# Performance work log

Measured on AMD Instinct MI355X. Metric: run time of the kernel, lower is better.

The kernel has to match this reference:

```python
import jax, jax.numpy as jnp
import numpy as np

SPAN = 20
REPEAT = 90


def setup_inputs() -> dict:
    key = jax.random.key(0)
    k1, k2 = jax.random.split(key)
    B, C, H, W = 4, 1, 512, 512
    pred = jax.random.normal(k1, (B, C, H, W), dtype=jnp.float32)
    gt = jax.random.normal(k2, (B, C, H, W), dtype=jnp.float32)
    # random offsets: magnitude in [1, span], random sign (matches np.random logic in torch module)
    rng = np.random.default_rng(0)
    mag_h = rng.integers(1, SPAN + 1, size=REPEAT)
    mag_w = rng.integers(1, SPAN + 1, size=REPEAT)
    sign_h = np.where(rng.uniform(size=REPEAT) > 0.5, -1, 1)
    sign_w = np.where(rng.uniform(size=REPEAT) > 0.5, -1, 1)
    h_offsets = jnp.asarray(mag_h * sign_h, dtype=jnp.int32)
    w_offsets = jnp.asarray(mag_w * sign_w, dtype=jnp.int32)
    return {"pred": pred, "gt": gt, "h_offsets": h_offsets, "w_offsets": w_offsets}


def _relative_depth(x, h_offsets, w_offsets):
    """x: [B,C,H,W] -> [B,Hb,Wb,R*C] stack of base-block minus shifted-block diffs."""
    B, C, H, W = x.shape
    Hb, Wb = H - 2 * SPAN, W - 2 * SPAN
    base = jax.lax.dynamic_slice(x, (0, 0, SPAN, SPAN), (B, C, Hb, Wb))

    def one_shift(h, w):
        shifted = jax.lax.dynamic_slice(x, (0, 0, SPAN + h, SPAN + w), (B, C, Hb, Wb))
        return base - shifted

    rd = jax.vmap(one_shift)(h_offsets, w_offsets)          # [R,B,C,Hb,Wb]
    R = rd.shape[0]
    rd = jnp.transpose(rd, (1, 0, 2, 3, 4)).reshape(B, R * C, Hb, Wb)  # concat along channel
    return jnp.transpose(rd, (0, 2, 3, 1))                   # [B,Hb,Wb,R*C]


def _l2_normalize(rd):
    norm = jnp.linalg.norm(rd, axis=-1, keepdims=True)
    norm = jnp.where(norm == 0, jnp.ones_like(norm), norm)
    return rd / norm


def reference(pred, gt, h_offsets, w_offsets):
    pred_rd = _l2_normalize(_relative_depth(pred, h_offsets, w_offsets))
    gt_rd = _l2_normalize(_relative_depth(gt, h_offsets, w_offsets))
    return jnp.mean(jnp.abs(pred_rd - gt_rd))
```

## Files before the change

kernel.cpp:

```cpp
#include <hip/hip_runtime.h>
#include <hip/hip_fp16.h>

#define SPAN 20
#define REPEAT 90


constexpr int W  = 512;
constexpr int Wb = 472;
constexpr int TJ = 64;
constexpr int TI = 8;
constexpr int TW = TJ + 2 * SPAN;
constexpr int TH = TI + 2 * SPAN;

__global__ __launch_bounds__(256) void rd_loss_kernel(
    const float* __restrict__ pred, const float* __restrict__ gt,
    const int* __restrict__ hoff, const int* __restrict__ woff,
    float* __restrict__ out)
{
    __shared__ __half2 tile[TH * TW];
    __shared__ float wsum[4];

    const int t  = threadIdx.x;
    const int bx = blockIdx.x;
    const int by = blockIdx.y;
    const int b  = blockIdx.z;
    const int I0 = by * TI;
    const int J0 = bx * TJ;

    const float* pb_ = pred + b * (W * W);
    const float* gb_ = gt   + b * (W * W);

    for (int e = t; e < TH * TW; e += 256) {
        const int row = e / TW;
        const int col = e - row * TW;
        const int gr  = I0 + row;
        int gc        = J0 + col; gc = gc < 511 ? gc : 511;
        const int gi  = gr * W + gc;
        tile[e] = __floats2half2_rn(pb_[gi], gb_[gi]);
    }
    __syncthreads();

    const int jp = t & 31;
    const int ii = t >> 5;
    const int jj = 2 * jp;
    const int j0 = J0 + jj;

    const int base0 = (SPAN + ii) * TW + (SPAN + jj);
    const __half2 c0 = tile[base0];
    const __half2 c1 = tile[base0 + 1];

    __half2 d0[REPEAT], d1[REPEAT];
    __half2 sA0 = __floats2half2_rn(0.f, 0.f), sB0 = sA0;
    __half2 sA1 = sA0, sB1 = sA0;
    #pragma unroll
    for (int r = 0; r < REPEAT; ++r) {
        const int off = hoff[r] * TW + woff[r];
        const __half2 v0 = tile[base0 + off];
        const __half2 v1 = tile[base0 + off + 1];
        d0[r] = __hsub2(c0, v0);
        d1[r] = __hsub2(c1, v1);
        if (r & 1) { sB0 = __hfma2(d0[r], d0[r], sB0); sB1 = __hfma2(d1[r], d1[r], sB1); }
        else       { sA0 = __hfma2(d0[r], d0[r], sA0); sA1 = __hfma2(d1[r], d1[r], sA1); }
    }
    const float ssp0 = __half2float(__low2half(sA0))  + __half2float(__low2half(sB0));
    const float ssg0 = __half2float(__high2half(sA0)) + __half2float(__high2half(sB0));
    const float ssp1 = __half2float(__low2half(sA1))  + __half2float(__low2half(sB1));
    const float ssg1 = __half2float(__high2half(sA1)) + __half2float(__high2half(sB1));

    const float invp0 = (ssp0 == 0.f) ? 1.f : rsqrtf(ssp0);
    const float invg0 = (ssg0 == 0.f) ? 1.f : rsqrtf(ssg0);
    const float invp1 = (ssp1 == 0.f) ? 1.f : rsqrtf(ssp1);
    const float invg1 = (ssg1 == 0.f) ? 1.f : rsqrtf(ssg1);

    const __half nr0 = __float2half(-(invg0 / invp0));
    const __half nr1 = __float2half(-(invg1 / invp1));

    __half aA0 = __float2half(0.f), aB0 = aA0, aA1 = aA0, aB1 = aA0;
    #pragma unroll
    for (int r = 0; r < REPEAT; ++r) {
        const __half s0 = __hfma(nr0, __high2half(d0[r]), __low2half(d0[r]));
        const __half s1 = __hfma(nr1, __high2half(d1[r]), __low2half(d1[r]));
        if (r & 1) { aB0 = __hadd(aB0, __habs(s0)); aB1 = __hadd(aB1, __habs(s1)); }
        else       { aA0 = __hadd(aA0, __habs(s0)); aA1 = __hadd(aA1, __habs(s1)); }
    }
    const float l0 = invp0 * (__half2float(aA0) + __half2float(aB0));
    const float l1 = invp1 * (__half2float(aA1) + __half2float(aB1));

    float lsum = ((j0 < Wb) ? l0 : 0.f) + ((j0 + 1 < Wb) ? l1 : 0.f);

    #pragma unroll
    for (int o = 32; o > 0; o >>= 1) lsum += __shfl_down(lsum, o, 64);

    const int lane = t & 63;
    const int wid  = t >> 6;
    if (lane == 0) wsum[wid] = lsum;
    __syncthreads();

    if (t == 0) {
        const float s = wsum[0] + wsum[1] + wsum[2] + wsum[3];
        constexpr float scale = 1.0f / (4.0f * 472.0f * 472.0f * 90.0f);
        atomicAdd(out, s * scale);
    }
}

extern "C" void kernel_launch(void* const* d_in, const int* in_sizes, int n_in,
                              void* d_out, int out_size, void* d_ws, size_t ws_size,
                              hipStream_t stream) {
    const float* pred = (const float*)d_in[0];
    const float* gt   = (const float*)d_in[1];
    const int* hoff   = (const int*)d_in[2];
    const int* woff   = (const int*)d_in[3];
    float* out = (float*)d_out;

    hipMemsetAsync(out, 0, sizeof(float), stream);

    dim3 grid(8, 59, 4);
    rd_loss_kernel<<<grid, 256, 0, stream>>>(pred, gt, hoff, woff, out);
}
```

Before: 53.48 us.

## Use dual-parity packed shared planes and recompute diffs instead of holding them in registers

The shared tile is stored as two planes of packed column pairs, one aligned to even shifts and one to odd shifts, so each shift needs a single 64-bit LDS load instead of two 32-bit loads. The 180 per-thread diff registers are dropped. The second pass reloads from LDS and recomputes the diffs, and launch bounds now request 4 blocks per CU for higher occupancy. Global loads become float2 vectors. The cost is twice the shared memory footprint and a second full pass of LDS reads.

After: 88.23 us. 65.0% more time.

```diff
diff --git a/kernel.cpp b/kernel.cpp
--- a/kernel.cpp
+++ b/kernel.cpp
@@ -11,13 +11,17 @@
 constexpr int TI = 8;
 constexpr int TW = TJ + 2 * SPAN;
 constexpr int TH = TI + 2 * SPAN;
+constexpr int QW = TW / 2;
+constexpr int PLANE = TH * QW;
 
-__global__ __launch_bounds__(256) void rd_loss_kernel(
+union Q { __half2 h[2]; uint2 u; };
+
+__global__ __launch_bounds__(256, 4) void rd_loss_kernel(
     const float* __restrict__ pred, const float* __restrict__ gt,
     const int* __restrict__ hoff, const int* __restrict__ woff,
     float* __restrict__ out)
 {
-    __shared__ __half2 tile[TH * TW];
+    __shared__ uint2 plane[2][PLANE];
     __shared__ float wsum[4];
 
     const int t  = threadIdx.x;
@@ -30,37 +34,47 @@
     const float* pb_ = pred + b * (W * W);
     const float* gb_ = gt   + b * (W * W);
 
-    for (int e = t; e < TH * TW; e += 256) {
-        const int row = e / TW;
-        const int col = e - row * TW;
+    for (int e = t; e < PLANE; e += 256) {
+        const int row = e / QW;
+        const int q   = e - row * QW;
         const int gr  = I0 + row;
-        int gc        = J0 + col; gc = gc < 511 ? gc : 511;
-        const int gi  = gr * W + gc;
-        tile[e] = __floats2half2_rn(pb_[gi], gb_[gi]);
+        int c0 = J0 + 2 * q;  c0 = c0 < 510 ? c0 : 510;
+        int c2 = c0 + 2;      c2 = c2 < 510 ? c2 : 510;
+        const float2 pLo = *(const float2*)(pb_ + gr * W + c0);
+        const float2 gLo = *(const float2*)(gb_ + gr * W + c0);
+        const float2 pHi = *(const float2*)(pb_ + gr * W + c2);
+        const float2 gHi = *(const float2*)(gb_ + gr * W + c2);
+        const __half2 h0 = __floats2half2_rn(pLo.x, gLo.x);
+        const __half2 h1 = __floats2half2_rn(pLo.y, gLo.y);
+        const __half2 h2 = __floats2half2_rn(pHi.x, gHi.x);
+        Q u0; u0.h[0] = h0; u0.h[1] = h1;
+        Q u1; u1.h[0] = h1; u1.h[1] = h2;
+        plane[0][e] = u0.u;
+        plane[1][e] = u1.u;
     }
     __syncthreads();
 
-    const int jp = t & 31;
-    const int ii = t >> 5;
-    const int jj = 2 * jp;
-    const int j0 = J0 + jj;
+    const int jp  = t & 31;
+    const int row = t >> 5;
+    const bool ok0 = (J0 + 2 * jp)     < Wb;
+    const bool ok1 = (J0 + 2 * jp + 1) < Wb;
 
-    const int base0 = (SPAN + ii) * TW + (SPAN + jj);
-    const __half2 c0 = tile[base0];
-    const __half2 c1 = tile[base0 + 1];
+    const int lanebase = row * QW + jp;
+    Q cc; cc.u = plane[0][(SPAN + row) * QW + (SPAN / 2 + jp)];
+    const __half2 c0 = cc.h[0], c1 = cc.h[1];
 
-    __half2 d0[REPEAT], d1[REPEAT];
     __half2 sA0 = __floats2half2_rn(0.f, 0.f), sB0 = sA0;
     __half2 sA1 = sA0, sB1 = sA0;
     #pragma unroll
     for (int r = 0; r < REPEAT; ++r) {
-        const int off = hoff[r] * TW + woff[r];
-        const __half2 v0 = tile[base0 + off];
-        const __half2 v1 = tile[base0 + off + 1];
-        d0[r] = __hsub2(c0, v0);
-        d1[r] = __hsub2(c1, v1);
-        if (r & 1) { sB0 = __hfma2(d0[r], d0[r], sB0); sB1 = __hfma2(d1[r], d1[r], sB1); }
-        else       { sA0 = __hfma2(d0[r], d0[r], sA0); sA1 = __hfma2(d1[r], d1[r], sA1); }
+        const int ho = hoff[r], wo = woff[r];
+        const int pi = wo & 1;
+        const int uo = (SPAN + ho) * QW + ((SPAN + wo - pi) >> 1);
+        Q vv; vv.u = plane[pi][lanebase + uo];
+        const __half2 d0 = __hsub2(c0, vv.h[0]);
+        const __half2 d1 = __hsub2(c1, vv.h[1]);
+        if (r & 1) { sB0 = __hfma2(d0, d0, sB0); sB1 = __hfma2(d1, d1, sB1); }
+        else       { sA0 = __hfma2(d0, d0, sA0); sA1 = __hfma2(d1, d1, sA1); }
     }
     const float ssp0 = __half2float(__low2half(sA0))  + __half2float(__low2half(sB0));
     const float ssg0 = __half2float(__high2half(sA0)) + __half2float(__high2half(sB0));
@@ -75,18 +89,24 @@
     const __half nr0 = __float2half(-(invg0 / invp0));
     const __half nr1 = __float2half(-(invg1 / invp1));
 
-    __half aA0 = __float2half(0.f), aB0 = aA0, aA1 = aA0, aB1 = aA0;
+    __half a0A = __float2half(0.f), a0B = a0A, a1A = a0A, a1B = a0A;
     #pragma unroll
     for (int r = 0; r < REPEAT; ++r) {
-        const __half s0 = __hfma(nr0, __high2half(d0[r]), __low2half(d0[r]));
-        const __half s1 = __hfma(nr1, __high2half(d1[r]), __low2half(d1[r]));
-        if (r & 1) { aB0 = __hadd(aB0, __habs(s0)); aB1 = __hadd(aB1, __habs(s1)); }
-        else       { aA0 = __hadd(aA0, __habs(s0)); aA1 = __hadd(aA1, __habs(s1)); }
+        const int ho = hoff[r], wo = woff[r];
+        const int pi = wo & 1;
+        const int uo = (SPAN + ho) * QW + ((SPAN + wo - pi) >> 1);
+        Q vv; vv.u = plane[pi][lanebase + uo];
+        const __half2 d0 = __hsub2(c0, vv.h[0]);
+        const __half2 d1 = __hsub2(c1, vv.h[1]);
+        const __half s0 = __hfma(nr0, __high2half(d0), __low2half(d0));
+        const __half s1 = __hfma(nr1, __high2half(d1), __low2half(d1));
+        if (r & 1) { a0B = __hadd(a0B, __habs(s0)); a1B = __hadd(a1B, __habs(s1)); }
+        else       { a0A = __hadd(a0A, __habs(s0)); a1A = __hadd(a1A, __habs(s1)); }
     }
-    const float l0 = invp0 * (__half2float(aA0) + __half2float(aB0));
-    const float l1 = invp1 * (__half2float(aA1) + __half2float(aB1));
+    const float l0 = invp0 * (__half2float(a0A) + __half2float(a0B));
+    const float l1 = invp1 * (__half2float(a1A) + __half2float(a1B));
 
-    float lsum = ((j0 < Wb) ? l0 : 0.f) + ((j0 + 1 < Wb) ? l1 : 0.f);
+    float lsum = (ok0 ? l0 : 0.f) + (ok1 ? l1 : 0.f);
 
     #pragma unroll
     for (int o = 32; o > 0; o >>= 1) lsum += __shfl_down(lsum, o, 64);
```
